# Performance work log

Hardware: AMD Instinct MI355X
Metric: run time of the kernel (lower is better)

Reference implementation:

```python
import jax, jax.numpy as jnp
import numpy as np

NHEAD = 8

def layernorm(x, g, b, eps=1e-5):
    mu = x.mean(-1, keepdims=True)
    var = ((x - mu) ** 2).mean(-1, keepdims=True)
    return (x - mu) / jnp.sqrt(var + eps) * g + b

def linear_attention(q, k, v, eps=1e-6):
    # LoFTR kernelized linear attention: phi(x) = elu(x) + 1
    Q = jax.nn.elu(q) + 1.0          # [n, l, h, d]
    K = jax.nn.elu(k) + 1.0          # [n, s, h, d]
    s_len = v.shape[1]
    KV = jnp.einsum("nshd,nshv->nhdv", K, v / s_len)
    Z = 1.0 / (jnp.einsum("nlhd,nhd->nlh", Q, K.sum(axis=1)) + eps)
    return jnp.einsum("nlhd,nhdv,nlh->nlhv", Q, KV, Z) * s_len

def _block(x_base, q, k, v, Wm, W1, W2, g1, b1, g2, b2):
    bs, L, h, dh = q.shape
    msg = linear_attention(q, k, v).reshape(bs, L, h * dh)
    msg = layernorm(msg @ Wm, g1, b1)
    hcat = jnp.concatenate([x_base, msg], axis=2)          # [bs, L, 2*d]
    out = jax.nn.relu(hcat @ W1) @ W2
    return layernorm(out, g2, b2)

def setup_inputs() -> dict:
    key = jax.random.key(0)
    ks = jax.random.split(key, 8)
    bs, L, S, d = 8, 4800, 4800, 256
    w = lambda k, i, o: jax.random.normal(k, (i, o), jnp.float32) * 0.02
    return {
        "x": jax.random.normal(ks[0], (bs, L, d), jnp.float32),
        "source": jax.random.normal(ks[1], (bs, S, d), jnp.float32),
        "Wq": w(ks[2], d, d), "Wk": w(ks[3], d, d), "Wv": w(ks[4], d, d),
        "Wm": w(ks[5], d, d),
        "W1": w(ks[6], 2 * d, 2 * d), "W2": w(ks[7], 2 * d, d),
        "g1": jnp.ones((d,), jnp.float32), "b1": jnp.zeros((d,), jnp.float32),
        "g2": jnp.ones((d,), jnp.float32), "b2": jnp.zeros((d,), jnp.float32),
    }

def reference(x, source, Wq, Wk, Wv, Wm, W1, W2, g1, b1, g2, b2):
    bs, L, d = x.shape
    h = NHEAD
    dh = d // h
    q = (x @ Wq).reshape(bs, L, h, dh)
    k = (source @ Wk).reshape(bs, -1, h, dh)
    v = (source @ Wv).reshape(bs, -1, h, dh)
    # permute-then-view reinterpretations, exactly as in the torch code
    p13 = lambda t: t.transpose(0, 1, 3, 2).reshape(bs, -1, h, dh)  # permute(0,1,3,2)
    p21 = lambda t: t.transpose(0, 2, 1, 3).reshape(bs, -1, h, dh)  # permute(0,2,1,3)
    p32 = lambda t: t.transpose(0, 3, 2, 1).reshape(bs, -1, h, dh)  # permute(0,3,2,1)
    blk = lambda xb, qq, kk, vv: _block(xb, qq, kk, vv, Wm, W1, W2, g1, b1, g2, b2)
    m = blk(x, q, k, v)
    m3 = blk(x, p13(q), p13(k), p13(v))
    x_mid = x + 0.5 * (m + m3)
    m1 = blk(x_mid, p21(q), p21(k), p21(v))
    m2 = blk(x_mid, p32(q), p32(k), p32(v))
    return x_mid + 0.5 * (m1 + m2)
```

## Files before the change

kernel.cpp:

```cpp
#include <hip/hip_runtime.h>
#include <type_traits>
#include <cstdint>
#include <cstddef>

#define L_SEQ 4800
#define DMODEL 256
#define BS 8
#define MROWS (BS*L_SEQ)
#define PERBATCH (L_SEQ*DMODEL)
#define KVSET 67584

typedef __attribute__((ext_vector_type(8))) short bfrag8;
typedef __attribute__((ext_vector_type(4))) float floatx4;

__device__ __forceinline__ float bf2f(unsigned short u){
  union { unsigned int i; float f; } x; x.i = ((unsigned int)u) << 16; return x.f;
}
__device__ __forceinline__ unsigned short f2bf(float f){
  union { float f; unsigned int i; } x; x.f = f;
  x.i += 0x7fff + ((x.i >> 16) & 1);
  return (unsigned short)(x.i >> 16);
}
__device__ __forceinline__ float phi(float x){
  return x > 0.f ? x + 1.f : __expf(x);
}
__device__ __forceinline__ void gll16(const void* g, void* l){
  __builtin_amdgcn_global_load_lds((const __attribute__((address_space(1))) unsigned int*)g,
      (__attribute__((address_space(3))) unsigned int*)l, 16, 0, 0);
}

template<typename TC, bool RELU>
__global__ __launch_bounds__(256) void gemm_mfma(const unsigned short* __restrict__ A,
                                                 const unsigned short* __restrict__ Bt,
                                                 TC* __restrict__ C, int M, int N, int K){
  __shared__ unsigned short Al[2][4096];
  __shared__ unsigned short Bl[2][4096];
  const int tid  = threadIdx.x;
  const int lane = tid & 63;
  const int wave = tid >> 6;
  const int row0 = blockIdx.y << 7;
  const int col0 = blockIdx.x << 7;
  const int wr0  = (wave & 1) << 6;
  const int wc0  = (wave >> 1) << 6;
  const int m = lane & 15, q = lane >> 4;
  const int sw = (m >> 1) & 3;

  floatx4 acc[4][4] = {};

  const int u0 = tid, u1 = tid + 256;
  const int r0 = u0 >> 2, s0 = u0 & 3;
  const int r1 = u1 >> 2, s1 = u1 & 3;

  auto stage = [&](int k0, int b){
    gll16(A  + (size_t)(row0 + r0)*K + k0 + ((s0 ^ ((r0 >> 1) & 3)) << 3), Al[b] + (size_t)u0*8);
    gll16(A  + (size_t)(row0 + r1)*K + k0 + ((s1 ^ ((r1 >> 1) & 3)) << 3), Al[b] + (size_t)u1*8);
    gll16(Bt + (size_t)(col0 + r0)*K + k0 + ((s0 ^ ((r0 >> 1) & 3)) << 3), Bl[b] + (size_t)u0*8);
    gll16(Bt + (size_t)(col0 + r1)*K + k0 + ((s1 ^ ((r1 >> 1) & 3)) << 3), Bl[b] + (size_t)u1*8);
  };

  stage(0, 0);
  const int nk = K >> 5;
  for (int ks = 0; ks < nk; ks++){
    asm volatile("s_waitcnt vmcnt(0) lgkmcnt(0)" ::: "memory");
    __builtin_amdgcn_s_barrier();
    asm volatile("" ::: "memory");
    if (ks < nk - 1) stage((ks + 1) << 5, (ks + 1) & 1);
    const unsigned short* ab = Al[ks & 1];
    const unsigned short* bb = Bl[ks & 1];
    bfrag8 af[4], bf[4];
    #pragma unroll
    for (int t = 0; t < 4; t++){
      af[t] = *(const bfrag8*)(ab + (size_t)(wr0 + t*16 + m)*32 + ((q ^ sw) << 3));
      bf[t] = *(const bfrag8*)(bb + (size_t)(wc0 + t*16 + m)*32 + ((q ^ sw) << 3));
    }
    #pragma unroll
    for (int mt = 0; mt < 4; mt++)
      #pragma unroll
      for (int nt = 0; nt < 4; nt++)
        acc[mt][nt] = __builtin_amdgcn_mfma_f32_16x16x32_bf16(af[mt], bf[nt], acc[mt][nt], 0, 0, 0);
  }

  #pragma unroll
  for (int mt = 0; mt < 4; mt++){
    #pragma unroll
    for (int nt = 0; nt < 4; nt++){
      const int col  = col0 + wc0 + nt*16 + m;
      const int rowb = row0 + wr0 + mt*16 + q*4;
      #pragma unroll
      for (int i = 0; i < 4; i++){
        float v = acc[mt][nt][i];
        if (RELU) v = v > 0.f ? v : 0.f;
        if constexpr (std::is_same<TC,float>::value) C[(size_t)(rowb+i)*N + col] = v;
        else                                         C[(size_t)(rowb+i)*N + col] = f2bf(v);
      }
    }
  }
}

template<int MODE>
__global__ __launch_bounds__(256) void gemm_ln(const unsigned short* __restrict__ A,
                                               const unsigned short* __restrict__ Bt,
                                               const float* __restrict__ g,
                                               const float* __restrict__ b,
                                               unsigned short* __restrict__ outb,
                                               float* __restrict__ outf,
                                               int K, int add){
  __shared__ unsigned short Ab[2][2048];
  __shared__ unsigned short Bb[2][8192];
  __shared__ float2 LNp[64][4];
  __shared__ float2 LNmu[64];
  const int tid = threadIdx.x;
  const int wv = tid >> 6, lane = tid & 63;
  const int m = lane & 15, qd = lane >> 4;
  const int sw = (m >> 1) & 3;
  const int row0 = blockIdx.x << 6;

  const int ra = tid >> 2, sa = tid & 3;

  auto stage = [&](int k0, int bsel){
    gll16(A + (size_t)(row0 + ra)*K + k0 + ((sa ^ ((ra >> 1) & 3)) << 3), Ab[bsel] + (size_t)tid*8);
    #pragma unroll
    for (int i = 0; i < 4; i++){
      int u = (i << 8) + tid;
      int c = u >> 2, s = u & 3;
      gll16(Bt + (size_t)c*K + k0 + ((s ^ ((c >> 1) & 3)) << 3), Bb[bsel] + (size_t)u*8);
    }
  };

  floatx4 acc[4][4] = {};
  stage(0, 0);
  const int nk = K >> 5;
  for (int ks = 0; ks < nk; ks++){
    asm volatile("s_waitcnt vmcnt(0) lgkmcnt(0)" ::: "memory");
    __builtin_amdgcn_s_barrier();
    asm volatile("" ::: "memory");
    if (ks < nk - 1) stage((ks + 1) << 5, (ks + 1) & 1);
    const unsigned short* ab = Ab[ks & 1];
    const unsigned short* bb = Bb[ks & 1];
    bfrag8 af[4], bf[4];
    #pragma unroll
    for (int t = 0; t < 4; t++){
      af[t] = *(const bfrag8*)(ab + (size_t)(t*16 + m)*32 + ((qd ^ sw) << 3));
      bf[t] = *(const bfrag8*)(bb + (size_t)(wv*64 + t*16 + m)*32 + ((qd ^ sw) << 3));
    }
    #pragma unroll
    for (int mt = 0; mt < 4; mt++)
      #pragma unroll
      for (int nt = 0; nt < 4; nt++)
        acc[mt][nt] = __builtin_amdgcn_mfma_f32_16x16x32_bf16(af[mt], bf[nt], acc[mt][nt], 0, 0, 0);
  }

  #pragma unroll
  for (int mt = 0; mt < 4; mt++)
    #pragma unroll
    for (int i = 0; i < 4; i++){
      float s = 0.f, q = 0.f;
      #pragma unroll
      for (int nt = 0; nt < 4; nt++){ float v = acc[mt][nt][i]; s += v; q += v*v; }
      #pragma unroll
      for (int o = 1; o < 16; o <<= 1){ s += __shfl_xor(s, o, 64); q += __shfl_xor(q, o, 64); }
      if (m == 0) LNp[mt*16 + qd*4 + i][wv] = make_float2(s, q);
    }
  __syncthreads();
  if (tid < 64){
    float2 p0 = LNp[tid][0], p1 = LNp[tid][1], p2 = LNp[tid][2], p3 = LNp[tid][3];
    float S = p0.x + p1.x + p2.x + p3.x;
    float Q = p0.y + p1.y + p2.y + p3.y;
    float mean = S * (1.f/256.f);
    float var  = Q * (1.f/256.f) - mean*mean;
    LNmu[tid] = make_float2(mean, rsqrtf(var + 1e-5f));
  }
  __syncthreads();

  float gv[4], bv[4];
  #pragma unroll
  for (int nt = 0; nt < 4; nt++){ int col = wv*64 + nt*16 + m; gv[nt] = g[col]; bv[nt] = b[col]; }
  #pragma unroll
  for (int mt = 0; mt < 4; mt++)
    #pragma unroll
    for (int i = 0; i < 4; i++){
      int row = mt*16 + qd*4 + i;
      float2 ms = LNmu[row];
      const size_t rowg = row0 + row;
      #pragma unroll
      for (int nt = 0; nt < 4; nt++){
        int col = wv*64 + nt*16 + m;
        float y = (acc[mt][nt][i] - ms.x) * ms.y * gv[nt] + bv[nt];
        if constexpr (MODE == 0){
          outb[rowg*512 + 256 + col] = f2bf(y);
        } else {
          float* p = outf + rowg*256 + col;
          if (add) y += *p;
          *p = y;
        }
      }
    }
}

__global__ __launch_bounds__(256) void wconv(const float* __restrict__ W, unsigned short* __restrict__ Wt,
                                             int kshift, int N){
  int idx = blockIdx.x*256 + threadIdx.x;
  int kk = idx & ((1 << kshift) - 1);
  int nn = idx >> kshift;
  Wt[idx] = f2bf(W[(size_t)kk*N + nn]);
}
__global__ __launch_bounds__(256) void conv_bf16(const float* __restrict__ in, unsigned short* __restrict__ out){
  int i = blockIdx.x*256 + threadIdx.x;
  float4 v = ((const float4*)in)[i];
  ushort4 o; o.x = f2bf(v.x); o.y = f2bf(v.y); o.z = f2bf(v.z); o.w = f2bf(v.w);
  ((ushort4*)out)[i] = o;
}

__global__ __launch_bounds__(256) void permute1(const unsigned short* __restrict__ sA, unsigned short* __restrict__ dA,
                                                const unsigned short* __restrict__ sB, unsigned short* __restrict__ dB){
  const unsigned short* s = blockIdx.z ? sB : sA;
  unsigned short*       d = blockIdx.z ? dB : dA;
  __shared__ unsigned short tile[1024];
  const int t = threadIdx.x;
  const size_t base = (size_t)blockIdx.x * 1024;
  #pragma unroll
  for (int i = 0; i < 4; i++) tile[i*256 + t] = s[base + i*256 + t];
  __syncthreads();
  const int pg = ((t & 7) << 5) + (t >> 3);
  #pragma unroll
  for (int i = 0; i < 4; i++) d[base + i*256 + t] = tile[i*256 + pg];
}

__global__ __launch_bounds__(256) void permute2(const unsigned short* __restrict__ sA, unsigned short* __restrict__ dA,
                                                const unsigned short* __restrict__ sB, unsigned short* __restrict__ dB){
  const unsigned short* s = blockIdx.z ? sB : sA;
  unsigned short*       d = blockIdx.z ? dB : dA;
  __shared__ unsigned short tile[64*256];
  const int t = threadIdx.x;
  const int rr0 = blockIdx.x * 64;
  const size_t boff = (size_t)blockIdx.y * PERBATCH;
  #pragma unroll
  for (int i = 0; i < 16; i++){
    int u = i*256 + t;
    *(ushort4*)&tile[u*4] = *(const ushort4*)&s[boff + (size_t)rr0*256 + (size_t)u*4];
  }
  __syncthreads();
  #pragma unroll
  for (int i = 0; i < 8; i++){
    #pragma unroll
    for (int w = 0; w < 2; w++){
      int u = w*256 + t;
      int rr = u >> 3, c4 = (u & 7) << 2;
      ushort4 v = *(const ushort4*)&tile[rr*256 + i*32 + c4];
      *(ushort4*)&d[boff + (size_t)i*153600 + (size_t)rr0*32 + (size_t)u*4] = v;
    }
  }
}

__global__ __launch_bounds__(256) void permute3(const unsigned short* __restrict__ sA, unsigned short* __restrict__ dA,
                                                const unsigned short* __restrict__ sB, unsigned short* __restrict__ dB){
  const unsigned short* s = blockIdx.z ? sB : sA;
  unsigned short*       d = blockIdx.z ? dB : dA;
  __shared__ unsigned short tile[64*258];
  const int t = threadIdx.x;
  const int ll0 = blockIdx.x * 64;
  const size_t boff = (size_t)blockIdx.y * PERBATCH;
  #pragma unroll
  for (int i = 0; i < 32; i++){
    int u = i*256 + t;
    int row = u >> 7, col = (u & 127) << 1;
    *(ushort2*)&tile[row*258 + col] = *(const ushort2*)&s[boff + (size_t)(ll0+row)*256 + col];
  }
  __syncthreads();
  const int cw = t >> 6;
  const int ll = t & 63;
  #pragma unroll
  for (int cc = 0; cc < 256; cc += 4){
    int c = cc + cw;
    int sigma = ((c & 31) << 3) + (c >> 5);
    d[boff + (size_t)sigma*4800 + ll0 + ll] = tile[ll*258 + c];
  }
}

__global__ __launch_bounds__(256) void attn_stats(const unsigned short* __restrict__ kq,
                                                  const unsigned short* __restrict__ vq,
                                                  float* __restrict__ KV, float* __restrict__ Ksum){
  const int chunk = blockIdx.x, h = blockIdx.y, n = blockIdx.z;
  const int t = threadIdx.x;
  const int d = t >> 3;
  const int w4 = (t & 7) << 2;
  const size_t boff = (size_t)n * PERBATCH;
  __shared__ float kb[8][32], vb[8][32];
  const int lr = t >> 5, lj = t & 31;
  float a0=0.f, a1=0.f, a2=0.f, a3=0.f, ks=0.f;
  const int s0 = chunk * 240;
  for (int s = s0; s < s0 + 240; s += 8){
    int srci = (s + lr)*256 + (h << 5) + lj;
    kb[lr][lj] = phi(bf2f(kq[boff + srci]));
    vb[lr][lj] = bf2f(vq[boff + srci]);
    __syncthreads();
    #pragma unroll
    for (int r = 0; r < 8; r++){
      float kd = kb[r][d];
      ks += kd;
      a0 += kd * vb[r][w4+0];
      a1 += kd * vb[r][w4+1];
      a2 += kd * vb[r][w4+2];
      a3 += kd * vb[r][w4+3];
    }
    __syncthreads();
  }
  float* kvp = KV + (size_t)((((n<<3)+h)<<5) + d)*32 + w4;
  atomicAdd(kvp+0, a0);
  atomicAdd(kvp+1, a1);
  atomicAdd(kvp+2, a2);
  atomicAdd(kvp+3, a3);
  if ((t & 7) == 0) atomicAdd(Ksum + (((n<<3)+h)<<5) + d, ks);
}

__global__ __launch_bounds__(256) void attn_apply(const unsigned short* __restrict__ qq,
                                                  const float* __restrict__ KV,
                                                  const float* __restrict__ Ksum,
                                                  unsigned short* __restrict__ msg){
  __shared__ float kvs[8192];
  __shared__ float kss[256];
  __shared__ float Qs[4096];
  const int t = threadIdx.x;
  const int n = blockIdx.y;
  const int row0 = blockIdx.x << 4;
  const size_t boff = (size_t)n * PERBATCH;

  #pragma unroll
  for (int i = 0; i < 32; i++) kvs[i*256 + t] = KV[(size_t)n*8192 + i*256 + t];
  kss[t] = Ksum[n*256 + t];
  #pragma unroll
  for (int r = 0; r < 16; r++)
    Qs[r*256 + t] = phi(bf2f(qq[boff + (size_t)(row0 + r)*256 + t]));
  __syncthreads();

  const int h = t >> 5, w = t & 31;
  const float* kvh = kvs + h*1024;
  const float* ksh = kss + h*32;
  float acc[16], den[16];
  #pragma unroll
  for (int r = 0; r < 16; r++){ acc[r] = 0.f; den[r] = 1e-6f; }

  #pragma unroll
  for (int d4 = 0; d4 < 8; d4++){
    const float k0 = kvh[(d4*4+0)*32 + w];
    const float k1 = kvh[(d4*4+1)*32 + w];
    const float k2 = kvh[(d4*4+2)*32 + w];
    const float k3 = kvh[(d4*4+3)*32 + w];
    const float s0 = ksh[d4*4+0], s1 = ksh[d4*4+1], s2 = ksh[d4*4+2], s3 = ksh[d4*4+3];
    #pragma unroll
    for (int r = 0; r < 16; r++){
      float4 qv = *(const float4*)&Qs[r*256 + h*32 + d4*4];
      acc[r] += qv.x*k0 + qv.y*k1 + qv.z*k2 + qv.w*k3;
      den[r] += qv.x*s0 + qv.y*s1 + qv.z*s2 + qv.w*s3;
    }
  }
  #pragma unroll
  for (int r = 0; r < 16; r++)
    msg[boff + (size_t)(row0 + r)*256 + t] = f2bf(acc[r]/den[r]);
}

__global__ __launch_bounds__(256) void fill_hcat(const float* __restrict__ x, unsigned short* __restrict__ hcat){
  size_t i = (size_t)blockIdx.x*256 + threadIdx.x;
  hcat[(i >> 8)*512 + (i & 255)] = f2bf(x[i]);
}
__global__ __launch_bounds__(256) void xmid_k(const float* __restrict__ x, const float* __restrict__ macc,
                                              float* __restrict__ xmid, unsigned short* __restrict__ hcat){
  size_t i = (size_t)blockIdx.x*256 + threadIdx.x;
  float v = x[i] + 0.5f*macc[i];
  xmid[i] = v;
  hcat[(i >> 8)*512 + (i & 255)] = f2bf(v);
}
__global__ __launch_bounds__(256) void final_k(float* __restrict__ out, const float* __restrict__ macc){
  size_t i = (size_t)blockIdx.x*256 + threadIdx.x;
  out[i] = out[i] + 0.5f*macc[i];
}
__global__ __launch_bounds__(256) void zero_k(float* __restrict__ p, int n){
  int i = blockIdx.x*256 + threadIdx.x;
  if (i < n) p[i] = 0.f;
}

extern "C" void kernel_launch(void* const* d_in, const int* in_sizes, int n_in,
                              void* d_out, int out_size, void* d_ws, size_t ws_size,
                              hipStream_t stream){
  const float* x   = (const float*)d_in[0];
  const float* src = (const float*)d_in[1];
  const float* Wq  = (const float*)d_in[2];
  const float* Wk  = (const float*)d_in[3];
  const float* Wv  = (const float*)d_in[4];
  const float* Wm  = (const float*)d_in[5];
  const float* W1  = (const float*)d_in[6];
  const float* W2  = (const float*)d_in[7];
  const float* g1  = (const float*)d_in[8];
  const float* b1  = (const float*)d_in[9];
  const float* g2  = (const float*)d_in[10];
  const float* b2  = (const float*)d_in[11];
  float* out = (float*)d_out;

  char* ws = (char*)d_ws;
  size_t off = 0;
  auto alloc = [&](size_t bytes) -> void* {
    void* p = ws + off;
    off += (bytes + 255) & ~(size_t)255;
    return p;
  };
  unsigned short* qB    = (unsigned short*)alloc((size_t)MROWS*256*2);
  unsigned short* kB    = (unsigned short*)alloc((size_t)MROWS*256*2);
  unsigned short* vB    = (unsigned short*)alloc((size_t)MROWS*256*2);
  unsigned short* hcatB = (unsigned short*)alloc((size_t)MROWS*512*2);
  float* t1   = (float*)alloc((size_t)MROWS*256*4);
  float* macc = (float*)alloc((size_t)MROWS*256*4);
  float* KV4  = (float*)alloc((size_t)4*KVSET*4);
  unsigned short* WqT = (unsigned short*)alloc((size_t)256*256*2);
  unsigned short* WkT = (unsigned short*)alloc((size_t)256*256*2);
  unsigned short* WvT = (unsigned short*)alloc((size_t)256*256*2);
  unsigned short* WmT = (unsigned short*)alloc((size_t)256*256*2);
  unsigned short* W1T = (unsigned short*)alloc((size_t)512*512*2);
  unsigned short* W2T = (unsigned short*)alloc((size_t)256*512*2);
  (void)ws_size; (void)in_sizes; (void)n_in; (void)out_size;

  unsigned short* msgB  = kB;
  unsigned short* hidB  = kB;
  unsigned short* srcbf = (unsigned short*)t1;
  unsigned short* xbf   = srcbf + (size_t)MROWS*256;
  unsigned short* qP    = (unsigned short*)t1;
  unsigned short* kP    = (unsigned short*)macc;
  unsigned short* vP    = kP + (size_t)MROWS*256;
  float* xmid = out;

  const dim3 blk(256);

  wconv<<<dim3(256),  blk, 0, stream>>>(Wq, WqT, 8, 256);
  wconv<<<dim3(256),  blk, 0, stream>>>(Wk, WkT, 8, 256);
  wconv<<<dim3(256),  blk, 0, stream>>>(Wv, WvT, 8, 256);
  wconv<<<dim3(256),  blk, 0, stream>>>(Wm, WmT, 8, 256);
  wconv<<<dim3(1024), blk, 0, stream>>>(W1, W1T, 9, 512);
  wconv<<<dim3(512),  blk, 0, stream>>>(W2, W2T, 9, 256);
  conv_bf16<<<dim3(9600), blk, 0, stream>>>(src, srcbf);
  conv_bf16<<<dim3(9600), blk, 0, stream>>>(x,   xbf);

  gemm_mfma<unsigned short, false><<<dim3(2,300), blk, 0, stream>>>(xbf,   WqT, qB, MROWS, 256, 256);
  gemm_mfma<unsigned short, false><<<dim3(2,300), blk, 0, stream>>>(srcbf, WkT, kB, MROWS, 256, 256);
  gemm_mfma<unsigned short, false><<<dim3(2,300), blk, 0, stream>>>(srcbf, WvT, vB, MROWS, 256, 256);

  zero_k<<<dim3(1056), blk, 0, stream>>>(KV4, 4*KVSET);
  attn_stats<<<dim3(20,8,8), blk, 0, stream>>>(kB, vB, KV4 + 0*KVSET, KV4 + 0*KVSET + 65536);
  permute1<<<dim3(9600,1,2), blk, 0, stream>>>(kB, kP, vB, vP);
  attn_stats<<<dim3(20,8,8), blk, 0, stream>>>(kP, vP, KV4 + 1*KVSET, KV4 + 1*KVSET + 65536);
  permute2<<<dim3(75,8,2),  blk, 0, stream>>>(kB, kP, vB, vP);
  attn_stats<<<dim3(20,8,8), blk, 0, stream>>>(kP, vP, KV4 + 2*KVSET, KV4 + 2*KVSET + 65536);
  permute3<<<dim3(75,8,2),  blk, 0, stream>>>(kB, kP, vB, vP);
  attn_stats<<<dim3(20,8,8), blk, 0, stream>>>(kP, vP, KV4 + 3*KVSET, KV4 + 3*KVSET + 65536);

  fill_hcat<<<dim3(MROWS), blk, 0, stream>>>(x, hcatB);

  auto run_block = [&](int mode, int add){
    const float* KV   = KV4 + (size_t)mode*KVSET;
    const float* Ksum = KV + 65536;
    const unsigned short* qsrc = qB;
    if (mode == 1){ permute1<<<dim3(9600,1,1), blk, 0, stream>>>(qB, qP, nullptr, nullptr); qsrc = qP; }
    else if (mode == 2){ permute2<<<dim3(75,8,1), blk, 0, stream>>>(qB, qP, nullptr, nullptr); qsrc = qP; }
    else if (mode == 3){ permute3<<<dim3(75,8,1), blk, 0, stream>>>(qB, qP, nullptr, nullptr); qsrc = qP; }
    attn_apply<<<dim3(300,BS), blk, 0, stream>>>(qsrc, KV, Ksum, msgB);
    gemm_ln<0><<<dim3(600), blk, 0, stream>>>(msgB, WmT, g1, b1, hcatB, nullptr, 256, 0);
    gemm_mfma<unsigned short, true><<<dim3(4,300), blk, 0, stream>>>(hcatB, W1T, hidB, MROWS, 512, 512);
    gemm_ln<1><<<dim3(600), blk, 0, stream>>>(hidB, W2T, g2, b2, nullptr, macc, 512, add);
  };

  run_block(0, 0);
  run_block(1, 1);
  xmid_k<<<dim3(MROWS), blk, 0, stream>>>(x, macc, xmid, hcatB);
  run_block(2, 0);
  run_block(3, 1);
  final_k<<<dim3(MROWS), blk, 0, stream>>>(out, macc);
}
```

Baseline: 1.011 ms.

## Pair attention blocks, split-source W1 GEMM, and single-buffered wide-K LN GEMM

Removes the concatenated hcat buffer. A new W1 GEMM reads the first K half from the bf16 x/x_mid buffer and the second half from the message buffer, which drops fill_hcat and the strided half-row writes. Blocks are processed in pairs, so both attention messages go through one gemm_ln launch with a 2-D grid before the two W1/W2 passes. The LN GEMM now stages 64-wide K slices with a single buffer and two barriers per step instead of double buffering. This may expose load latency, since compute no longer overlaps the next slice's loads.

```diff
diff --git a/kernel.cpp b/kernel.cpp
--- a/kernel.cpp
+++ b/kernel.cpp
@@ -97,16 +97,88 @@
   }
 }
 
+__global__ __launch_bounds__(256) void gemm_w1(const unsigned short* __restrict__ Axc,
+                                               const unsigned short* __restrict__ Amsg,
+                                               const unsigned short* __restrict__ Bt,
+                                               unsigned short* __restrict__ C){
+  __shared__ unsigned short Al[2][4096];
+  __shared__ unsigned short Bl[2][4096];
+  const int tid  = threadIdx.x;
+  const int lane = tid & 63;
+  const int wave = tid >> 6;
+  const int row0 = blockIdx.y << 7;
+  const int col0 = blockIdx.x << 7;
+  const int wr0  = (wave & 1) << 6;
+  const int wc0  = (wave >> 1) << 6;
+  const int m = lane & 15, q = lane >> 4;
+  const int sw = (m >> 1) & 3;
+  const int K = 512;
+
+  floatx4 acc[4][4] = {};
+
+  const int u0 = tid, u1 = tid + 256;
+  const int r0 = u0 >> 2, s0 = u0 & 3;
+  const int r1 = u1 >> 2, s1 = u1 & 3;
+
+  auto stage = [&](int ks, int b){
+    const int k0 = ks << 5;
+    const unsigned short* As = (ks < 8) ? Axc : Amsg;
+    const int kk = k0 & 255;
+    gll16(As + (size_t)(row0 + r0)*256 + kk + ((s0 ^ ((r0 >> 1) & 3)) << 3), Al[b] + (size_t)u0*8);
+    gll16(As + (size_t)(row0 + r1)*256 + kk + ((s1 ^ ((r1 >> 1) & 3)) << 3), Al[b] + (size_t)u1*8);
+    gll16(Bt + (size_t)(col0 + r0)*K + k0 + ((s0 ^ ((r0 >> 1) & 3)) << 3), Bl[b] + (size_t)u0*8);
+    gll16(Bt + (size_t)(col0 + r1)*K + k0 + ((s1 ^ ((r1 >> 1) & 3)) << 3), Bl[b] + (size_t)u1*8);
+  };
+
+  stage(0, 0);
+  for (int ks = 0; ks < 16; ks++){
+    asm volatile("s_waitcnt vmcnt(0) lgkmcnt(0)" ::: "memory");
+    __builtin_amdgcn_s_barrier();
+    asm volatile("" ::: "memory");
+    if (ks < 15) stage(ks + 1, (ks + 1) & 1);
+    const unsigned short* ab = Al[ks & 1];
+    const unsigned short* bb = Bl[ks & 1];
+    bfrag8 af[4], bf[4];
+    #pragma unroll
+    for (int t = 0; t < 4; t++){
+      af[t] = *(const bfrag8*)(ab + (size_t)(wr0 + t*16 + m)*32 + ((q ^ sw) << 3));
+      bf[t] = *(const bfrag8*)(bb + (size_t)(wc0 + t*16 + m)*32 + ((q ^ sw) << 3));
+    }
+    #pragma unroll
+    for (int mt = 0; mt < 4; mt++)
+      #pragma unroll
+      for (int nt = 0; nt < 4; nt++)
+        acc[mt][nt] = __builtin_amdgcn_mfma_f32_16x16x32_bf16(af[mt], bf[nt], acc[mt][nt], 0, 0, 0);
+  }
+
+  #pragma unroll
+  for (int mt = 0; mt < 4; mt++){
+    #pragma unroll
+    for (int nt = 0; nt < 4; nt++){
+      const int col  = col0 + wc0 + nt*16 + m;
+      const int rowb = row0 + wr0 + mt*16 + q*4;
+      #pragma unroll
+      for (int i = 0; i < 4; i++){
+        float v = acc[mt][nt][i];
+        v = v > 0.f ? v : 0.f;
+        C[(size_t)(rowb+i)*512 + col] = f2bf(v);
+      }
+    }
+  }
+}
+
 template<int MODE>
-__global__ __launch_bounds__(256) void gemm_ln(const unsigned short* __restrict__ A,
-                                               const unsigned short* __restrict__ Bt,
-                                               const float* __restrict__ g,
-                                               const float* __restrict__ b,
-                                               unsigned short* __restrict__ outb,
-                                               float* __restrict__ outf,
-                                               int K, int add){
-  __shared__ unsigned short Ab[2][2048];
-  __shared__ unsigned short Bb[2][8192];
+__global__ __launch_bounds__(256) void gemm_lnv2(const unsigned short* __restrict__ A0,
+                                                 const unsigned short* __restrict__ A1,
+                                                 const unsigned short* __restrict__ Bt,
+                                                 const float* __restrict__ g,
+                                                 const float* __restrict__ b,
+                                                 unsigned short* __restrict__ ob0,
+                                                 unsigned short* __restrict__ ob1,
+                                                 float* __restrict__ of,
+                                                 int K, int add){
+  __shared__ unsigned short Ab[4096];
+  __shared__ unsigned short Bb[16384];
   __shared__ float2 LNp[64][4];
   __shared__ float2 LNmu[64];
   const int tid = threadIdx.x;
@@ -114,40 +186,49 @@
   const int m = lane & 15, qd = lane >> 4;
   const int sw = (m >> 1) & 3;
   const int row0 = blockIdx.x << 6;
-
-  const int ra = tid >> 2, sa = tid & 3;
-
-  auto stage = [&](int k0, int bsel){
-    gll16(A + (size_t)(row0 + ra)*K + k0 + ((sa ^ ((ra >> 1) & 3)) << 3), Ab[bsel] + (size_t)tid*8);
-    #pragma unroll
-    for (int i = 0; i < 4; i++){
+  const unsigned short* A = (MODE == 0 && blockIdx.y) ? A1 : A0;
+  unsigned short* ob = (MODE == 0 && blockIdx.y) ? ob1 : ob0;
+
+  floatx4 acc[4][4] = {};
+  const int nsteps = K >> 6;
+  for (int o = 0; o < nsteps; o++){
+    const int k0 = o << 6;
+    #pragma unroll
+    for (int i = 0; i < 2; i++){
       int u = (i << 8) + tid;
-      int c = u >> 2, s = u & 3;
-      gll16(Bt + (size_t)c*K + k0 + ((s ^ ((c >> 1) & 3)) << 3), Bb[bsel] + (size_t)u*8);
-    }
-  };
-
-  floatx4 acc[4][4] = {};
-  stage(0, 0);
-  const int nk = K >> 5;
-  for (int ks = 0; ks < nk; ks++){
-    asm volatile("s_waitcnt vmcnt(0) lgkmcnt(0)" ::: "memory");
-    __builtin_amdgcn_s_barrier();
-    asm volatile("" ::: "memory");
-    if (ks < nk - 1) stage((ks + 1) << 5, (ks + 1) & 1);
-    const unsigned short* ab = Ab[ks & 1];
-    const unsigned short* bb = Bb[ks & 1];
-    bfrag8 af[4], bf[4];
-    #pragma unroll
-    for (int t = 0; t < 4; t++){
-      af[t] = *(const bfrag8*)(ab + (size_t)(t*16 + m)*32 + ((qd ^ sw) << 3));
-      bf[t] = *(const bfrag8*)(bb + (size_t)(wv*64 + t*16 + m)*32 + ((qd ^ sw) << 3));
-    }
-    #pragma unroll
-    for (int mt = 0; mt < 4; mt++)
-      #pragma unroll
-      for (int nt = 0; nt < 4; nt++)
-        acc[mt][nt] = __builtin_amdgcn_mfma_f32_16x16x32_bf16(af[mt], bf[nt], acc[mt][nt], 0, 0, 0);
+      int r = (u & 255) >> 2, s = u & 3, h = u >> 8;
+      gll16(A + (size_t)(row0 + r)*K + k0 + h*32 + ((s ^ ((r >> 1) & 3)) << 3),
+            Ab + (size_t)u*8);
+    }
+    #pragma unroll
+    for (int i = 0; i < 8; i++){
+      int u = (i << 8) + tid;
+      int c = (u & 1023) >> 2, s = u & 3, h = u >> 10;
+      gll16(Bt + (size_t)c*K + k0 + h*32 + ((s ^ ((c >> 1) & 3)) << 3),
+            Bb + (size_t)u*8);
+    }
+    asm volatile("s_waitcnt vmcnt(0)" ::: "memory");
+    __syncthreads();
+    #pragma unroll
+    for (int j = 0; j < 2; j++){
+      bfrag8 af[4], bf[4];
+      #pragma unroll
+      for (int mt = 0; mt < 4; mt++){
+        int r = mt*16 + m;
+        af[mt] = *(const bfrag8*)(Ab + (size_t)j*2048 + (size_t)r*32 + ((qd ^ sw) << 3));
+      }
+      #pragma unroll
+      for (int nt = 0; nt < 4; nt++){
+        int c = wv*64 + nt*16 + m;
+        bf[nt] = *(const bfrag8*)(Bb + (size_t)j*8192 + (size_t)c*32 + ((qd ^ sw) << 3));
+      }
+      #pragma unroll
+      for (int mt = 0; mt < 4; mt++)
+        #pragma unroll
+        for (int nt = 0; nt < 4; nt++)
+          acc[mt][nt] = __builtin_amdgcn_mfma_f32_16x16x32_bf16(af[mt], bf[nt], acc[mt][nt], 0, 0, 0);
+    }
+    __syncthreads();
   }
 
   #pragma unroll
@@ -187,9 +268,9 @@
         int col = wv*64 + nt*16 + m;
         float y = (acc[mt][nt][i] - ms.x) * ms.y * gv[nt] + bv[nt];
         if constexpr (MODE == 0){
-          outb[rowg*512 + 256 + col] = f2bf(y);
+          ob[rowg*256 + col] = f2bf(y);
         } else {
-          float* p = outf + rowg*256 + col;
+          float* p = of + rowg*256 + col;
           if (add) y += *p;
           *p = y;
         }
@@ -359,16 +440,12 @@
     msg[boff + (size_t)(row0 + r)*256 + t] = f2bf(acc[r]/den[r]);
 }
 
-__global__ __launch_bounds__(256) void fill_hcat(const float* __restrict__ x, unsigned short* __restrict__ hcat){
-  size_t i = (size_t)blockIdx.x*256 + threadIdx.x;
-  hcat[(i >> 8)*512 + (i & 255)] = f2bf(x[i]);
-}
 __global__ __launch_bounds__(256) void xmid_k(const float* __restrict__ x, const float* __restrict__ macc,
-                                              float* __restrict__ xmid, unsigned short* __restrict__ hcat){
+                                              float* __restrict__ xmid, unsigned short* __restrict__ xcbf){
   size_t i = (size_t)blockIdx.x*256 + threadIdx.x;
   float v = x[i] + 0.5f*macc[i];
   xmid[i] = v;
-  hcat[(i >> 8)*512 + (i & 255)] = f2bf(v);
+  xcbf[i] = f2bf(v);
 }
 __global__ __launch_bounds__(256) void final_k(float* __restrict__ out, const float* __restrict__ macc){
   size_t i = (size_t)blockIdx.x*256 + threadIdx.x;
@@ -403,10 +480,10 @@
     off += (bytes + 255) & ~(size_t)255;
     return p;
   };
-  unsigned short* qB    = (unsigned short*)alloc((size_t)MROWS*256*2);
-  unsigned short* kB    = (unsigned short*)alloc((size_t)MROWS*256*2);
-  unsigned short* vB    = (unsigned short*)alloc((size_t)MROWS*256*2);
-  unsigned short* hcatB = (unsigned short*)alloc((size_t)MROWS*512*2);
+  unsigned short* qB   = (unsigned short*)alloc((size_t)MROWS*256*2);
+  unsigned short* kB   = (unsigned short*)alloc((size_t)MROWS*256*2);
+  unsigned short* vB   = (unsigned short*)alloc((size_t)MROWS*256*2);
+  unsigned short* mlnB = (unsigned short*)alloc((size_t)MROWS*512*2);
   float* t1   = (float*)alloc((size_t)MROWS*256*4);
   float* macc = (float*)alloc((size_t)MROWS*256*4);
   float* KV4  = (float*)alloc((size_t)4*KVSET*4);
@@ -418,13 +495,12 @@
   unsigned short* W2T = (unsigned short*)alloc((size_t)256*512*2);
   (void)ws_size; (void)in_sizes; (void)n_in; (void)out_size;
 
-  unsigned short* msgB  = kB;
-  unsigned short* hidB  = kB;
-  unsigned short* srcbf = (unsigned short*)t1;
-  unsigned short* xbf   = srcbf + (size_t)MROWS*256;
-  unsigned short* qP    = (unsigned short*)t1;
-  unsigned short* kP    = (unsigned short*)macc;
-  unsigned short* vP    = kP + (size_t)MROWS*256;
+  unsigned short* srcbf  = (unsigned short*)t1;
+  unsigned short* xcbf   = srcbf + (size_t)MROWS*256;
+  unsigned short* qP     = (unsigned short*)t1;
+  unsigned short* msgln0 = mlnB;
+  unsigned short* msgln1 = mlnB + (size_t)MROWS*256;
+  unsigned short* hid    = kB;
   float* xmid = out;
 
   const dim3 blk(256);
@@ -436,12 +512,14 @@
   wconv<<<dim3(1024), blk, 0, stream>>>(W1, W1T, 9, 512);
   wconv<<<dim3(512),  blk, 0, stream>>>(W2, W2T, 9, 256);
   conv_bf16<<<dim3(9600), blk, 0, stream>>>(src, srcbf);
-  conv_bf16<<<dim3(9600), blk, 0, stream>>>(x,   xbf);
-
-  gemm_mfma<unsigned short, false><<<dim3(2,300), blk, 0, stream>>>(xbf,   WqT, qB, MROWS, 256, 256);
+  conv_bf16<<<dim3(9600), blk, 0, stream>>>(x,   xcbf);
+
+  gemm_mfma<unsigned short, false><<<dim3(2,300), blk, 0, stream>>>(xcbf,  WqT, qB, MROWS, 256, 256);
   gemm_mfma<unsigned short, false><<<dim3(2,300), blk, 0, stream>>>(srcbf, WkT, kB, MROWS, 256, 256);
   gemm_mfma<unsigned short, false><<<dim3(2,300), blk, 0, stream>>>(srcbf, WvT, vB, MROWS, 256, 256);
 
+  unsigned short* kP = (unsigned short*)macc;
+  unsigned short* vP = kP + (size_t)MROWS*256;
   zero_k<<<dim3(1056), blk, 0, stream>>>(KV4, 4*KVSET);
   attn_stats<<<dim3(20,8,8), blk, 0, stream>>>(kB, vB, KV4 + 0*KVSET, KV4 + 0*KVSET + 65536);
   permute1<<<dim3(9600,1,2), blk, 0, stream>>>(kB, kP, vB, vP);
@@ -451,25 +529,28 @@
   permute3<<<dim3(75,8,2),  blk, 0, stream>>>(kB, kP, vB, vP);
   attn_stats<<<dim3(20,8,8), blk, 0, stream>>>(kP, vP, KV4 + 3*KVSET, KV4 + 3*KVSET + 65536);
 
-  fill_hcat<<<dim3(MROWS), blk, 0, stream>>>(x, hcatB);
-
-  auto run_block = [&](int mode, int add){
-    const float* KV   = KV4 + (size_t)mode*KVSET;
-    const float* Ksum = KV + 65536;
-    const unsigned short* qsrc = qB;
-    if (mode == 1){ permute1<<<dim3(9600,1,1), blk, 0, stream>>>(qB, qP, nullptr, nullptr); qsrc = qP; }
-    else if (mode == 2){ permute2<<<dim3(75,8,1), blk, 0, stream>>>(qB, qP, nullptr, nullptr); qsrc = qP; }
-    else if (mode == 3){ permute3<<<dim3(75,8,1), blk, 0, stream>>>(qB, qP, nullptr, nullptr); qsrc = qP; }
-    attn_apply<<<dim3(300,BS), blk, 0, stream>>>(qsrc, KV, Ksum, msgB);
-    gemm_ln<0><<<dim3(600), blk, 0, stream>>>(msgB, WmT, g1, b1, hcatB, nullptr, 256, 0);
-    gemm_mfma<unsigned short, true><<<dim3(4,300), blk, 0, stream>>>(hcatB, W1T, hidB, MROWS, 512, 512);
-    gemm_ln<1><<<dim3(600), blk, 0, stream>>>(hidB, W2T, g2, b2, nullptr, macc, 512, add);
+  auto run_pair = [&](int modeA, int modeB, int addA){
+    {
+      const float* KV   = KV4 + (size_t)modeA*KVSET;
+      const unsigned short* qsrc = qB;
+      if (modeA == 2){ permute2<<<dim3(75,8,1), blk, 0, stream>>>(qB, qP, nullptr, nullptr); qsrc = qP; }
+      attn_apply<<<dim3(300,BS), blk, 0, stream>>>(qsrc, KV, KV + 65536, kB);
+    }
+    {
+      const float* KV   = KV4 + (size_t)modeB*KVSET;
+      if (modeB == 1)      permute1<<<dim3(9600,1,1), blk, 0, stream>>>(qB, qP, nullptr, nullptr);
+      else                 permute3<<<dim3(75,8,1),   blk, 0, stream>>>(qB, qP, nullptr, nullptr);
+      attn_apply<<<dim3(300,BS), blk, 0, stream>>>(qP, KV, KV + 65536, vB);
+    }
+    gemm_lnv2<0><<<dim3(600,2), blk, 0, stream>>>(kB, vB, WmT, g1, b1, msgln0, msgln1, nullptr, 256, 0);
+    gemm_w1<<<dim3(4,300), blk, 0, stream>>>(xcbf, msgln0, W1T, hid);
+    gemm_lnv2<1><<<dim3(600,1), blk, 0, stream>>>(hid, nullptr, W2T, g2, b2, nullptr, nullptr, macc, 512, addA);
+    gemm_w1<<<dim3(4,300), blk, 0, stream>>>(xcbf, msgln1, W1T, hid);
+    gemm_lnv2<1><<<dim3(600,1), blk, 0, stream>>>(hid, nullptr, W2T, g2, b2, nullptr, nullptr, macc, 512, 1);
   };
 
-  run_block(0, 0);
-  run_block(1, 1);
-  xmid_k<<<dim3(MROWS), blk, 0, stream>>>(x, macc, xmid, hcatB);
-  run_block(2, 0);
-  run_block(3, 1);
+  run_pair(0, 1, 0);
+  xmid_k<<<dim3(MROWS), blk, 0, stream>>>(x, macc, xmid, xcbf);
+  run_pair(2, 3, 0);
   final_k<<<dim3(MROWS), blk, 0, stream>>>(out, macc);
 }
```

After: 979.9 us. 3.1% less time.
